# Kernel tuning notes

Measured on AMD Instinct MI355X. Metric: run time of the kernel, lower is better.

## Reference

```python
import jax, jax.numpy as jnp
import numpy as np

BS, D_IN, D_SP, K = 2048, 1024, 16384, 32
THRESH = 100.0


def setup_inputs() -> dict:
    key = jax.random.key(0)
    k0, k1, k2, k3, k4 = jax.random.split(key, 5)
    x = jax.random.normal(k0, (BS, D_IN), jnp.float32)
    W1 = jax.random.normal(k1, (D_SP, D_IN), jnp.float32) / np.sqrt(D_IN).astype(np.float32)
    W2 = jax.random.normal(k2, (D_IN, D_SP), jnp.float32) / np.sqrt(D_SP).astype(np.float32)
    bias_pre = jax.random.normal(k3, (D_IN,), jnp.float32) * 0.01
    last_activation = jax.random.randint(k4, (D_SP,), 0, 512).astype(jnp.float32)
    return {"x": x, "W1": W1, "W2": W2, "bias_pre": bias_pre, "last_activation": last_activation}


def reference(x, W1, W2, bias_pre, last_activation):
    bs = x.shape[0]
    # encoder: (x - b_pre) @ W1^T  -> [bs, D_SP]
    scores = (x - bias_pre) @ W1.T
    # global top-k over flattened (b d)
    flat = scores.reshape(-1)
    vals, idx = jax.lax.top_k(flat, K * bs)
    topk = jnp.zeros_like(flat).at[idx].set(vals).reshape(bs, D_SP)
    # dead-neuron bookkeeping: neurons active anywhere in batch reset to 0
    active = (topk != 0).any(axis=0)  # [D_SP]
    la = (last_activation + 1.0) * (1.0 - active.astype(last_activation.dtype))
    dead = la > THRESH  # [D_SP]
    # masked per-row top-2k over dead neurons only
    neg_inf = jnp.float32(-jnp.inf)
    dead_act = jnp.where(dead[None, :], scores, neg_inf)
    dvals, didx = jax.lax.top_k(dead_act, 2 * K)  # [bs, 2k]
    dvals = jnp.where(jnp.isinf(dvals), jnp.float32(0.0), dvals)
    dead_topk = jnp.zeros_like(scores).at[jnp.arange(bs)[:, None], didx].set(dvals)
    # decodes
    dead_recon = dead_topk @ W2.T
    recon = topk @ W2.T + bias_pre
    return recon, dead_recon
```

## Files before the change

### kernel.cpp

```cpp
#include <hip/hip_runtime.h>

#define BS    2048
#define DIN   1024
#define DSP   16384
#define NTOT  (BS * DSP)
#define NSEL  65536
#define TOPD  64
#define ROWCAP 256
#define TIECAP 8192
#define THRESHV 100.0f
#define U_LO  0xC0000000u
#define CANDCAP 1048576u

#define C_B1 0
#define C_NEED1 1
#define C_G1 2
#define C_B2 3
#define C_NEED2 4
#define C_G2 5
#define C_B3 6
#define C_NEED3 7
#define C_G3 8
#define C_USTAR 9
#define C_NTIE 10
#define C_TIECNT 11
#define C_DEADCNT 12
#define C_CANDCNT 13

#define OFF_CTRL   0u
#define OFF_H1     256u
#define OFF_H2     8448u
#define OFF_H3     16640u
#define OFF_ACT    20736u
#define OFF_RC     22784u
#define ZERO_BYTES 30976u
#define OFF_TIE    30976u
#define OFF_DCOLS  63744u
#define OFF_DRCNT  129280u
#define OFF_DRCOL  137472u
#define OFF_DRVAL  661760u
#define OFF_RCOLS  1186048u
#define OFF_RVALS  3283200u
#define OFF_XB     5380352u
#define OFF_CAND   OFF_XB
#define OFF_W2T    13768960u
#define OFF_SC     80877824u

__device__ __forceinline__ unsigned uflip(float f) {
    unsigned b = __float_as_uint(f);
    return (b & 0x80000000u) ? ~b : (b | 0x80000000u);
}
__device__ __forceinline__ float unflip(unsigned u) {
    unsigned b = (u & 0x80000000u) ? (u & 0x7FFFFFFFu) : ~u;
    return __uint_as_float(b);
}

__global__ void k_xb(const float* __restrict__ x, const float* __restrict__ bias,
                     float* __restrict__ xb) {
    int i = blockIdx.x * 256 + threadIdx.x;
    xb[i] = x[i] - bias[i & (DIN - 1)];
}

__global__ void k_transpose(const float* __restrict__ W2, float* __restrict__ W2T) {
    __shared__ float tile[32][33];
    int c0 = blockIdx.x * 32;
    int r0 = blockIdx.y * 32;
    int tx = threadIdx.x, ty = threadIdx.y;
#pragma unroll
    for (int q = 0; q < 4; q++) {
        int r = ty + q * 8;
        tile[r][tx] = W2[(size_t)(r0 + r) * DSP + c0 + tx];
    }
    __syncthreads();
#pragma unroll
    for (int q = 0; q < 4; q++) {
        int r = ty + q * 8;
        W2T[(size_t)(c0 + r) * DIN + r0 + tx] = tile[tx][r];
    }
}

#define LDP 132
__global__ __launch_bounds__(256, 2) void k_gemm(const float* __restrict__ A,
                                                 const float* __restrict__ Bm,
                                                 float* __restrict__ C) {
    __shared__ float As[16][LDP];
    __shared__ float Bs[16][LDP];
    const int tid = threadIdx.x;
    const int tx = tid & 15;
    const int ty = tid >> 4;
    const int row0 = blockIdx.y * 128;
    const int col0 = blockIdx.x * 128;

    const int r0l = tid >> 2;
    const int kq  = (tid & 3) << 2;
    const float* Ap0 = A  + (size_t)(row0 + r0l) * DIN + kq;
    const float* Ap1 = Ap0 + (size_t)64 * DIN;
    const float* Bp0 = Bm + (size_t)(col0 + r0l) * DIN + kq;
    const float* Bp1 = Bp0 + (size_t)64 * DIN;

    float acc[8][8];
#pragma unroll
    for (int i = 0; i < 8; i++)
#pragma unroll
        for (int j = 0; j < 8; j++) acc[i][j] = 0.0f;

    float4 pa0 = *(const float4*)(Ap0);
    float4 pa1 = *(const float4*)(Ap1);
    float4 pb0 = *(const float4*)(Bp0);
    float4 pb1 = *(const float4*)(Bp1);

    for (int k0 = 0; k0 < DIN; k0 += 16) {
        __syncthreads();
        As[kq + 0][r0l] = pa0.x; As[kq + 1][r0l] = pa0.y;
        As[kq + 2][r0l] = pa0.z; As[kq + 3][r0l] = pa0.w;
        As[kq + 0][r0l + 64] = pa1.x; As[kq + 1][r0l + 64] = pa1.y;
        As[kq + 2][r0l + 64] = pa1.z; As[kq + 3][r0l + 64] = pa1.w;
        Bs[kq + 0][r0l] = pb0.x; Bs[kq + 1][r0l] = pb0.y;
        Bs[kq + 2][r0l] = pb0.z; Bs[kq + 3][r0l] = pb0.w;
        Bs[kq + 0][r0l + 64] = pb1.x; Bs[kq + 1][r0l + 64] = pb1.y;
        Bs[kq + 2][r0l + 64] = pb1.z; Bs[kq + 3][r0l + 64] = pb1.w;
        __syncthreads();

        if (k0 + 16 < DIN) {
            pa0 = *(const float4*)(Ap0 + k0 + 16);
            pa1 = *(const float4*)(Ap1 + k0 + 16);
            pb0 = *(const float4*)(Bp0 + k0 + 16);
            pb1 = *(const float4*)(Bp1 + k0 + 16);
        }

#pragma unroll
        for (int kk = 0; kk < 16; kk++) {
            float a[8], b[8];
            *(float4*)&a[0] = *(const float4*)&As[kk][ty * 8];
            *(float4*)&a[4] = *(const float4*)&As[kk][ty * 8 + 4];
            *(float4*)&b[0] = *(const float4*)&Bs[kk][tx * 4];
            *(float4*)&b[4] = *(const float4*)&Bs[kk][64 + tx * 4];
#pragma unroll
            for (int i = 0; i < 8; i++)
#pragma unroll
                for (int j = 0; j < 8; j++)
                    acc[i][j] = fmaf(a[i], b[j], acc[i][j]);
        }
    }
#pragma unroll
    for (int i = 0; i < 8; i++) {
        int r = row0 + ty * 8 + i;
        float4 o0 = make_float4(acc[i][0], acc[i][1], acc[i][2], acc[i][3]);
        float4 o1 = make_float4(acc[i][4], acc[i][5], acc[i][6], acc[i][7]);
        *(float4*)&C[(size_t)r * DSP + col0 + tx * 4]      = o0;
        *(float4*)&C[(size_t)r * DSP + col0 + 64 + tx * 4] = o1;
    }
}

__global__ void k_hist1(const float4* __restrict__ s4, unsigned* __restrict__ h1,
                        uint2* __restrict__ cand, unsigned* __restrict__ ctrl) {
    __shared__ unsigned hl[2048];
    __shared__ uint2 lbuf[2048];
    __shared__ unsigned lcnt, lbase;
    for (int i = threadIdx.x; i < 2048; i += 256) hl[i] = 0;
    if (threadIdx.x == 0) lcnt = 0;
    __syncthreads();
    int stride = gridDim.x * blockDim.x;
    for (int t = blockIdx.x * blockDim.x + threadIdx.x; t < NTOT / 4; t += stride) {
        float4 v = s4[t];
        float vv[4] = {v.x, v.y, v.z, v.w};
#pragma unroll
        for (int e = 0; e < 4; e++) {
            unsigned u = uflip(vv[e]);
            if (u >= U_LO) {
                atomicAdd(&hl[u >> 21], 1u);
                unsigned p = atomicAdd(&lcnt, 1u);
                if (p < 2048u) {
                    lbuf[p] = make_uint2(u, (unsigned)(4 * t + e));
                } else {
                    unsigned g = atomicAdd(&ctrl[C_CANDCNT], 1u);
                    if (g < CANDCAP) cand[g] = make_uint2(u, (unsigned)(4 * t + e));
                }
            }
        }
    }
    __syncthreads();
    for (int i = threadIdx.x; i < 2048; i += 256)
        if (hl[i]) atomicAdd(&h1[i], hl[i]);
    if (threadIdx.x == 0) {
        unsigned m = min(lcnt, 2048u);
        lbase = atomicAdd(&ctrl[C_CANDCNT], m);
    }
    __syncthreads();
    unsigned m = min(lcnt, 2048u);
    for (unsigned i = threadIdx.x; i < m; i += 256) {
        unsigned dst = lbase + i;
        if (dst < CANDCAP) cand[dst] = lbuf[i];
    }
}

__global__ void k_hist2(const uint2* __restrict__ cand, const unsigned* __restrict__ ctrl,
                        unsigned* __restrict__ h2) {
    __shared__ unsigned hl[2048];
    for (int i = threadIdx.x; i < 2048; i += 256) hl[i] = 0;
    __syncthreads();
    unsigned n = min(ctrl[C_CANDCNT], CANDCAP);
    unsigned b1 = ctrl[C_B1];
    int stride = gridDim.x * blockDim.x;
    for (unsigned t = blockIdx.x * blockDim.x + threadIdx.x; t < n; t += stride) {
        unsigned u = cand[t].x;
        if ((u >> 21) == b1) atomicAdd(&hl[(u >> 10) & 0x7FFu], 1u);
    }
    __syncthreads();
    for (int i = threadIdx.x; i < 2048; i += 256)
        if (hl[i]) atomicAdd(&h2[i], hl[i]);
}

__global__ void k_hist3(const uint2* __restrict__ cand, const unsigned* __restrict__ ctrl,
                        unsigned* __restrict__ h3) {
    __shared__ unsigned hl[1024];
    for (int i = threadIdx.x; i < 1024; i += 256) hl[i] = 0;
    __syncthreads();
    unsigned n = min(ctrl[C_CANDCNT], CANDCAP);
    unsigned b12 = (ctrl[C_B1] << 11) | ctrl[C_B2];
    int stride = gridDim.x * blockDim.x;
    for (unsigned t = blockIdx.x * blockDim.x + threadIdx.x; t < n; t += stride) {
        unsigned u = cand[t].x;
        if ((u >> 10) == b12) atomicAdd(&hl[u & 0x3FFu], 1u);
    }
    __syncthreads();
    for (int i = threadIdx.x; i < 1024; i += 256)
        if (hl[i]) atomicAdd(&h3[i], hl[i]);
}

__global__ void k_scan(const unsigned* __restrict__ hist, int nbins,
                       const unsigned* __restrict__ need_ptr, unsigned need_const,
                       unsigned* __restrict__ out3) {
    __shared__ unsigned chs[256];
    int tid = threadIdx.x;
    int CH = nbins / 256;
    int base = tid * CH;
    unsigned s = 0;
    for (int i = 0; i < CH; i++) s += hist[base + i];
    chs[tid] = s;
    __syncthreads();
    unsigned suf = 0;
    for (int i = tid + 1; i < 256; i++) suf += chs[i];
    unsigned need = need_ptr ? *need_ptr : need_const;
    unsigned run = suf;
    for (int i = CH - 1; i >= 0; i--) {
        unsigned h = hist[base + i];
        if (run < need && run + h >= need) {
            out3[0] = (unsigned)(base + i);
            out3[1] = need - run;
            out3[2] = run;
        }
        run += h;
    }
}

__global__ void k_final(unsigned* ctrl) {
    ctrl[C_USTAR] = (ctrl[C_B1] << 21) | (ctrl[C_B2] << 10) | ctrl[C_B3];
    ctrl[C_NTIE] = ctrl[C_NEED3];
}

__device__ __forceinline__ void emit_sel(int t, float v, unsigned* row_count, int* row_cols,
                                         float* row_vals, unsigned* active) {
    int row = t >> 14;
    int col = t & (DSP - 1);
    unsigned s = atomicAdd(&row_count[row], 1u);
    if (s < ROWCAP) {
        row_cols[row * ROWCAP + s] = col;
        row_vals[row * ROWCAP + s] = v;
    }
    if (v != 0.0f) atomicOr(&active[col >> 5], 1u << (col & 31));
}

__global__ void k_select(const uint2* __restrict__ cand, unsigned* ctrl,
                         unsigned* row_count, int* row_cols, float* row_vals,
                         unsigned* active, int* tie_list) {
    unsigned n = min(ctrl[C_CANDCNT], CANDCAP);
    unsigned ustar = ctrl[C_USTAR];
    int stride = gridDim.x * blockDim.x;
    for (unsigned t = blockIdx.x * blockDim.x + threadIdx.x; t < n; t += stride) {
        unsigned u = cand[t].x;
        int idx = (int)cand[t].y;
        if (u > ustar) {
            emit_sel(idx, unflip(u), row_count, row_cols, row_vals, active);
        } else if (u == ustar) {
            unsigned p = atomicAdd(&ctrl[C_TIECNT], 1u);
            if (p < TIECAP) tie_list[p] = idx;
        }
    }
}

__global__ void k_ties(const float* __restrict__ scores, unsigned* ctrl,
                       const int* __restrict__ tie_list, unsigned* row_count,
                       int* row_cols, float* row_vals, unsigned* active) {
    int T = (int)min(ctrl[C_TIECNT], (unsigned)TIECAP);
    int need = (int)ctrl[C_NTIE];
    for (int e = threadIdx.x; e < T; e += 256) {
        int t = tie_list[e];
        bool take;
        if (T <= need) {
            take = true;
        } else {
            int rank = 0;
            for (int j = 0; j < T; j++) rank += (tie_list[j] < t);
            take = rank < need;
        }
        if (take) emit_sel(t, scores[t], row_count, row_cols, row_vals, active);
    }
}

__global__ void k_deadmask(const unsigned* __restrict__ active,
                           const float* __restrict__ lastact,
                           unsigned* ctrl, int* dead_cols) {
    int j = blockIdx.x * 256 + threadIdx.x;
    if (j < DSP) {
        bool act = (active[j >> 5] >> (j & 31)) & 1u;
        float la = (lastact[j] + 1.0f) * (act ? 0.0f : 1.0f);
        if (la > THRESHV) {
            unsigned p = atomicAdd(&ctrl[C_DEADCNT], 1u);
            dead_cols[p] = j;
        }
    }
}

#define MCAP 2048
__device__ __forceinline__ void bitonic_sort_asc(unsigned long long* keys, int tid, int n2) {
    for (int k = 2; k <= n2; k <<= 1) {
        for (int j = k >> 1; j > 0; j >>= 1) {
            __syncthreads();
            for (int t = tid; t < n2 / 2; t += 256) {
                int i = 2 * t - (t & (j - 1));
                int ixj = i | j;
                unsigned long long a = keys[i], b = keys[ixj];
                bool sw = ((i & k) == 0) ? (a > b) : (a < b);
                if (sw) { keys[i] = b; keys[ixj] = a; }
            }
        }
    }
    __syncthreads();
}

__global__ __launch_bounds__(256) void k_top64(const float* __restrict__ scores,
                                               const int* __restrict__ dead_cols,
                                               const unsigned* __restrict__ ctrl,
                                               int* drow_cnt, int* drow_cols,
                                               float* drow_vals) {
    __shared__ unsigned long long keys[MCAP];
    const int row = blockIdx.x;
    const int tid = threadIdx.x;
    const int D = (int)ctrl[C_DEADCNT];
    const float* srow = scores + (size_t)row * DSP;

    int n2 = 64;
    {
        int lim = (D < MCAP) ? D : MCAP;
        while (n2 < lim) n2 <<= 1;
    }
    int first = min(D, n2);
    for (int i = tid; i < n2; i += 256) {
        unsigned long long kv = 0ull;
        if (i < first) {
            int c = dead_cols[i];
            float v = srow[c];
            kv = ((unsigned long long)uflip(v) << 32) | (unsigned)(~(unsigned)c);
        }
        keys[i] = kv;
    }
    int processed = first;
    bitonic_sort_asc(keys, tid, n2);
    while (processed < D) {
        int c = min(D - processed, n2 - TOPD);
        for (int i = tid; i < n2 - TOPD; i += 256) {
            unsigned long long kv = 0ull;
            if (i < c) {
                int col = dead_cols[processed + i];
                float v = srow[col];
                kv = ((unsigned long long)uflip(v) << 32) | (unsigned)(~(unsigned)col);
            }
            keys[i] = kv;
        }
        processed += c;
        __syncthreads();
        bitonic_sort_asc(keys, tid, n2);
    }
    int n = min(D, TOPD);
    if (tid < n) {
        unsigned long long kv = keys[n2 - 1 - tid];
        unsigned uh = (unsigned)(kv >> 32);
        int col = (int)(~(unsigned)kv);
        drow_cols[row * TOPD + tid] = col;
        drow_vals[row * TOPD + tid] = unflip(uh);
    }
    if (tid == 0) drow_cnt[row] = n;
}

__global__ __launch_bounds__(256) void k_recon(const unsigned* __restrict__ row_count,
                                               const int* __restrict__ row_cols,
                                               const float* __restrict__ row_vals,
                                               const float* __restrict__ W2T,
                                               const float* __restrict__ bias,
                                               float* __restrict__ out) {
    int row = blockIdx.x, tid = threadIdx.x;
    int n = min((int)row_count[row], ROWCAP);
    float a0 = 0.f, a1 = 0.f, a2 = 0.f, a3 = 0.f;
    const int* rc = row_cols + row * ROWCAP;
    const float* rv = row_vals + row * ROWCAP;
    for (int s = 0; s < n; s++) {
        int k = rc[s];
        float v = rv[s];
        const float* w = W2T + (size_t)k * DIN;
        a0 = fmaf(v, w[tid], a0);       a1 = fmaf(v, w[tid + 256], a1);
        a2 = fmaf(v, w[tid + 512], a2); a3 = fmaf(v, w[tid + 768], a3);
    }
    float* o = out + (size_t)row * DIN;
    o[tid]       = a0 + bias[tid];
    o[tid + 256] = a1 + bias[tid + 256];
    o[tid + 512] = a2 + bias[tid + 512];
    o[tid + 768] = a3 + bias[tid + 768];
}

__global__ __launch_bounds__(256) void k_dead_recon(const int* __restrict__ drow_cnt,
                                                    const int* __restrict__ drow_cols,
                                                    const float* __restrict__ drow_vals,
                                                    const float* __restrict__ W2T,
                                                    float* __restrict__ out) {
    int row = blockIdx.x, tid = threadIdx.x;
    int n = drow_cnt[row];
    float a0 = 0.f, a1 = 0.f, a2 = 0.f, a3 = 0.f;
    const int* rc = drow_cols + row * TOPD;
    const float* rv = drow_vals + row * TOPD;
    for (int s = 0; s < n; s++) {
        int k = rc[s];
        float v = rv[s];
        const float* w = W2T + (size_t)k * DIN;
        a0 = fmaf(v, w[tid], a0);       a1 = fmaf(v, w[tid + 256], a1);
        a2 = fmaf(v, w[tid + 512], a2); a3 = fmaf(v, w[tid + 768], a3);
    }
    float* o = out + (size_t)row * DIN;
    o[tid] = a0; o[tid + 256] = a1; o[tid + 512] = a2; o[tid + 768] = a3;
}

extern "C" void kernel_launch(void* const* d_in, const int* in_sizes, int n_in,
                              void* d_out, int out_size, void* d_ws, size_t ws_size,
                              hipStream_t stream) {
    (void)in_sizes; (void)n_in; (void)out_size; (void)ws_size;
    const float* x        = (const float*)d_in[0];
    const float* W1       = (const float*)d_in[1];
    const float* W2       = (const float*)d_in[2];
    const float* bias     = (const float*)d_in[3];
    const float* lastact  = (const float*)d_in[4];
    float* out = (float*)d_out;

    char* wsb = (char*)d_ws;
    unsigned* ctrl      = (unsigned*)(wsb + OFF_CTRL);
    unsigned* h1        = (unsigned*)(wsb + OFF_H1);
    unsigned* h2        = (unsigned*)(wsb + OFF_H2);
    unsigned* h3        = (unsigned*)(wsb + OFF_H3);
    unsigned* active    = (unsigned*)(wsb + OFF_ACT);
    unsigned* row_count = (unsigned*)(wsb + OFF_RC);
    int*      tie_list  = (int*)(wsb + OFF_TIE);
    int*      dead_cols = (int*)(wsb + OFF_DCOLS);
    int*      drow_cnt  = (int*)(wsb + OFF_DRCNT);
    int*      drow_cols = (int*)(wsb + OFF_DRCOL);
    float*    drow_vals = (float*)(wsb + OFF_DRVAL);
    int*      row_cols  = (int*)(wsb + OFF_RCOLS);
    float*    row_vals  = (float*)(wsb + OFF_RVALS);
    float*    xb        = (float*)(wsb + OFF_XB);
    uint2*    cand      = (uint2*)(wsb + OFF_CAND);
    float*    W2T       = (float*)(wsb + OFF_W2T);
    float*    scores    = (float*)(wsb + OFF_SC);

    hipMemsetAsync(wsb, 0, ZERO_BYTES, stream);

    k_xb<<<BS * DIN / 256, 256, 0, stream>>>(x, bias, xb);
    k_transpose<<<dim3(DSP / 32, DIN / 32), dim3(32, 8), 0, stream>>>(W2, W2T);
    k_gemm<<<dim3(DSP / 128, BS / 128), 256, 0, stream>>>(xb, W1, scores);

    const float4* s4 = (const float4*)scores;
    k_hist1<<<1024, 256, 0, stream>>>(s4, h1, cand, ctrl);
    k_scan<<<1, 256, 0, stream>>>(h1, 2048, nullptr, NSEL, &ctrl[C_B1]);
    k_hist2<<<256, 256, 0, stream>>>(cand, ctrl, h2);
    k_scan<<<1, 256, 0, stream>>>(h2, 2048, &ctrl[C_NEED1], 0, &ctrl[C_B2]);
    k_hist3<<<256, 256, 0, stream>>>(cand, ctrl, h3);
    k_scan<<<1, 256, 0, stream>>>(h3, 1024, &ctrl[C_NEED2], 0, &ctrl[C_B3]);
    k_final<<<1, 1, 0, stream>>>(ctrl);

    k_select<<<256, 256, 0, stream>>>(cand, ctrl, row_count, row_cols, row_vals,
                                      active, tie_list);
    k_ties<<<1, 256, 0, stream>>>(scores, ctrl, tie_list, row_count, row_cols,
                                  row_vals, active);
    k_deadmask<<<DSP / 256, 256, 0, stream>>>(active, lastact, ctrl, dead_cols);
    k_top64<<<BS, 256, 0, stream>>>(scores, dead_cols, ctrl, drow_cnt, drow_cols,
                                    drow_vals);

    k_recon<<<BS, 256, 0, stream>>>(row_count, row_cols, row_vals, W2T, bias, out);
    k_dead_recon<<<BS, 256, 0, stream>>>(drow_cnt, drow_cols, drow_vals, W2T,
                                         out + (size_t)BS * DIN);
}
```

Measured before the change: 1.108 ms.

## Pre-transpose GEMM operands and double-buffer LDS with async global-to-LDS loads

The encoder GEMM now reads K-major operands: x minus bias is transposed into xbT and W1 into a scratch buffer. This lets each wave load contiguous 16-byte rows directly into LDS with global_load_lds, double-buffered so the next K-slice loads while the current one is computed. The W2 transpose moves after the top-k stages so it can reuse the same scratch buffer. The cost is two extra transpose passes over a 64MB weight matrix and the 8MB activations. The unpadded LDS layout may also cause bank conflicts.

```diff
diff --git a/kernel.cpp b/kernel.cpp
--- a/kernel.cpp
+++ b/kernel.cpp
@@ -55,13 +55,34 @@
     return __uint_as_float(b);
 }
 
-__global__ void k_xb(const float* __restrict__ x, const float* __restrict__ bias,
-                     float* __restrict__ xb) {
-    int i = blockIdx.x * 256 + threadIdx.x;
-    xb[i] = x[i] - bias[i & (DIN - 1)];
-}
-
-__global__ void k_transpose(const float* __restrict__ W2, float* __restrict__ W2T) {
+typedef __attribute__((address_space(3))) unsigned* lds_ptr_t;
+typedef const __attribute__((address_space(1))) unsigned* gbl_ptr_t;
+__device__ __forceinline__ void async_copy16(void* lds, const void* g) {
+    __builtin_amdgcn_global_load_lds((gbl_ptr_t)g, (lds_ptr_t)lds, 16, 0, 0);
+}
+
+__global__ void k_xbt(const float* __restrict__ x, const float* __restrict__ bias,
+                      float* __restrict__ xbT) {
+    __shared__ float tile[32][33];
+    int m0 = blockIdx.x * 32;
+    int k0 = blockIdx.y * 32;
+    int tx = threadIdx.x, ty = threadIdx.y;
+    float b = bias[k0 + tx];
+#pragma unroll
+    for (int q = 0; q < 4; q++) {
+        int m = ty + q * 8;
+        tile[m][tx] = x[(size_t)(m0 + m) * DIN + k0 + tx] - b;
+    }
+    __syncthreads();
+#pragma unroll
+    for (int q = 0; q < 4; q++) {
+        int k = ty + q * 8;
+        xbT[(size_t)(k0 + k) * BS + m0 + tx] = tile[tx][k];
+    }
+}
+
+__global__ void k_tr(const float* __restrict__ in, float* __restrict__ outp,
+                     int R, int Cc) {
     __shared__ float tile[32][33];
     int c0 = blockIdx.x * 32;
     int r0 = blockIdx.y * 32;
@@ -69,34 +90,36 @@
 #pragma unroll
     for (int q = 0; q < 4; q++) {
         int r = ty + q * 8;
-        tile[r][tx] = W2[(size_t)(r0 + r) * DSP + c0 + tx];
+        tile[r][tx] = in[(size_t)(r0 + r) * Cc + c0 + tx];
     }
     __syncthreads();
 #pragma unroll
     for (int q = 0; q < 4; q++) {
         int r = ty + q * 8;
-        W2T[(size_t)(c0 + r) * DIN + r0 + tx] = tile[tx][r];
-    }
-}
-
-#define LDP 132
-__global__ __launch_bounds__(256, 2) void k_gemm(const float* __restrict__ A,
-                                                 const float* __restrict__ Bm,
+        outp[(size_t)(c0 + r) * R + r0 + tx] = tile[tx][r];
+    }
+}
+
+#define BK 16
+__global__ __launch_bounds__(256, 2) void k_gemm(const float* __restrict__ AT,
+                                                 const float* __restrict__ BT,
                                                  float* __restrict__ C) {
-    __shared__ float As[16][LDP];
-    __shared__ float Bs[16][LDP];
+    __shared__ float As[2][BK][128];
+    __shared__ float Bs[2][BK][128];
     const int tid = threadIdx.x;
     const int tx = tid & 15;
     const int ty = tid >> 4;
     const int row0 = blockIdx.y * 128;
     const int col0 = blockIdx.x * 128;
-
-    const int r0l = tid >> 2;
-    const int kq  = (tid & 3) << 2;
-    const float* Ap0 = A  + (size_t)(row0 + r0l) * DIN + kq;
-    const float* Ap1 = Ap0 + (size_t)64 * DIN;
-    const float* Bp0 = Bm + (size_t)(col0 + r0l) * DIN + kq;
-    const float* Bp1 = Bp0 + (size_t)64 * DIN;
+    const int w    = tid >> 6;
+    const int lane = tid & 63;
+    const int lr   = lane >> 5;
+    const int lc   = (lane & 31) * 4;
+
+    const float* gA0 = AT + (size_t)(4 * w + 0 + lr) * BS + row0 + lc;
+    const float* gA1 = AT + (size_t)(4 * w + 2 + lr) * BS + row0 + lc;
+    const float* gB0 = BT + (size_t)(4 * w + 0 + lr) * DSP + col0 + lc;
+    const float* gB1 = BT + (size_t)(4 * w + 2 + lr) * DSP + col0 + lc;
 
     float acc[8][8];
 #pragma unroll
@@ -104,44 +127,40 @@
 #pragma unroll
         for (int j = 0; j < 8; j++) acc[i][j] = 0.0f;
 
-    float4 pa0 = *(const float4*)(Ap0);
-    float4 pa1 = *(const float4*)(Ap1);
-    float4 pb0 = *(const float4*)(Bp0);
-    float4 pb1 = *(const float4*)(Bp1);
-
-    for (int k0 = 0; k0 < DIN; k0 += 16) {
-        __syncthreads();
-        As[kq + 0][r0l] = pa0.x; As[kq + 1][r0l] = pa0.y;
-        As[kq + 2][r0l] = pa0.z; As[kq + 3][r0l] = pa0.w;
-        As[kq + 0][r0l + 64] = pa1.x; As[kq + 1][r0l + 64] = pa1.y;
-        As[kq + 2][r0l + 64] = pa1.z; As[kq + 3][r0l + 64] = pa1.w;
-        Bs[kq + 0][r0l] = pb0.x; Bs[kq + 1][r0l] = pb0.y;
-        Bs[kq + 2][r0l] = pb0.z; Bs[kq + 3][r0l] = pb0.w;
-        Bs[kq + 0][r0l + 64] = pb1.x; Bs[kq + 1][r0l + 64] = pb1.y;
-        Bs[kq + 2][r0l + 64] = pb1.z; Bs[kq + 3][r0l + 64] = pb1.w;
-        __syncthreads();
-
-        if (k0 + 16 < DIN) {
-            pa0 = *(const float4*)(Ap0 + k0 + 16);
-            pa1 = *(const float4*)(Ap1 + k0 + 16);
-            pb0 = *(const float4*)(Bp0 + k0 + 16);
-            pb1 = *(const float4*)(Bp1 + k0 + 16);
-        }
-
-#pragma unroll
-        for (int kk = 0; kk < 16; kk++) {
+    async_copy16(&As[0][4 * w + 0][0], gA0);
+    async_copy16(&As[0][4 * w + 2][0], gA1);
+    async_copy16(&Bs[0][4 * w + 0][0], gB0);
+    async_copy16(&Bs[0][4 * w + 2][0], gB1);
+    __syncthreads();
+
+    int p = 0;
+    for (int k0 = 0; k0 < DIN; k0 += BK) {
+        if (k0 + BK < DIN) {
+            int pn = p ^ 1;
+            size_t ka = (size_t)(k0 + BK) * BS;
+            size_t kb = (size_t)(k0 + BK) * DSP;
+            async_copy16(&As[pn][4 * w + 0][0], gA0 + ka);
+            async_copy16(&As[pn][4 * w + 2][0], gA1 + ka);
+            async_copy16(&Bs[pn][4 * w + 0][0], gB0 + kb);
+            async_copy16(&Bs[pn][4 * w + 2][0], gB1 + kb);
+        }
+#pragma unroll
+        for (int kk = 0; kk < BK; kk++) {
             float a[8], b[8];
-            *(float4*)&a[0] = *(const float4*)&As[kk][ty * 8];
-            *(float4*)&a[4] = *(const float4*)&As[kk][ty * 8 + 4];
-            *(float4*)&b[0] = *(const float4*)&Bs[kk][tx * 4];
-            *(float4*)&b[4] = *(const float4*)&Bs[kk][64 + tx * 4];
+            *(float4*)&a[0] = *(const float4*)&As[p][kk][ty * 8];
+            *(float4*)&a[4] = *(const float4*)&As[p][kk][ty * 8 + 4];
+            *(float4*)&b[0] = *(const float4*)&Bs[p][kk][tx * 4];
+            *(float4*)&b[4] = *(const float4*)&Bs[p][kk][64 + tx * 4];
 #pragma unroll
             for (int i = 0; i < 8; i++)
 #pragma unroll
                 for (int j = 0; j < 8; j++)
                     acc[i][j] = fmaf(a[i], b[j], acc[i][j]);
         }
-    }
+        __syncthreads();
+        p ^= 1;
+    }
+
 #pragma unroll
     for (int i = 0; i < 8; i++) {
         int r = row0 + ty * 8 + i;
@@ -464,16 +483,16 @@
     float*    drow_vals = (float*)(wsb + OFF_DRVAL);
     int*      row_cols  = (int*)(wsb + OFF_RCOLS);
     float*    row_vals  = (float*)(wsb + OFF_RVALS);
-    float*    xb        = (float*)(wsb + OFF_XB);
+    float*    xbT       = (float*)(wsb + OFF_XB);
     uint2*    cand      = (uint2*)(wsb + OFF_CAND);
-    float*    W2T       = (float*)(wsb + OFF_W2T);
+    float*    WT        = (float*)(wsb + OFF_W2T);
     float*    scores    = (float*)(wsb + OFF_SC);
 
     hipMemsetAsync(wsb, 0, ZERO_BYTES, stream);
 
-    k_xb<<<BS * DIN / 256, 256, 0, stream>>>(x, bias, xb);
-    k_transpose<<<dim3(DSP / 32, DIN / 32), dim3(32, 8), 0, stream>>>(W2, W2T);
-    k_gemm<<<dim3(DSP / 128, BS / 128), 256, 0, stream>>>(xb, W1, scores);
+    k_tr<<<dim3(DIN / 32, DSP / 32), dim3(32, 8), 0, stream>>>(W1, WT, DSP, DIN);
+    k_xbt<<<dim3(BS / 32, DIN / 32), dim3(32, 8), 0, stream>>>(x, bias, xbT);
+    k_gemm<<<dim3(DSP / 128, BS / 128), 256, 0, stream>>>(xbT, WT, scores);
 
     const float4* s4 = (const float4*)scores;
     k_hist1<<<1024, 256, 0, stream>>>(s4, h1, cand, ctrl);
@@ -492,7 +511,8 @@
     k_top64<<<BS, 256, 0, stream>>>(scores, dead_cols, ctrl, drow_cnt, drow_cols,
                                     drow_vals);
 
-    k_recon<<<BS, 256, 0, stream>>>(row_count, row_cols, row_vals, W2T, bias, out);
-    k_dead_recon<<<BS, 256, 0, stream>>>(drow_cnt, drow_cols, drow_vals, W2T,
+    k_tr<<<dim3(DSP / 32, DIN / 32), dim3(32, 8), 0, stream>>>(W2, WT, DIN, DSP);
+    k_recon<<<BS, 256, 0, stream>>>(row_count, row_cols, row_vals, WT, bias, out);
+    k_dead_recon<<<BS, 256, 0, stream>>>(drow_cnt, drow_cols, drow_vals, WT,
                                          out + (size_t)BS * DIN);
 }
```

Result: no change. 1.104 ms (-0.4%).
